# Performance work log

Hardware: AMD Instinct MI355X
Metric: run time of the kernel (lower is better)

## Reference

```python
import jax, jax.numpy as jnp
import numpy as np

B, S, D_IN, D_OUT = 4, 4096, 768, 768

def setup_inputs() -> dict:
    key = jax.random.key(0)
    k1, k2, k3, k4 = jax.random.split(key, 4)
    x = jax.random.normal(k1, (B, S, D_IN), dtype=jnp.float32)
    # Stored as [d_in, d_out]; torch Linear computes x @ W.T with W [d_out, d_in],
    # which is equivalent to x @ W_here for a fresh random init.
    Wq = jax.random.normal(k2, (D_IN, D_OUT), dtype=jnp.float32) * (1.0 / np.sqrt(D_IN))
    Wk = jax.random.normal(k3, (D_IN, D_OUT), dtype=jnp.float32) * (1.0 / np.sqrt(D_IN))
    Wv = jax.random.normal(k4, (D_IN, D_OUT), dtype=jnp.float32) * (1.0 / np.sqrt(D_IN))
    return {"x": x, "Wq": Wq, "Wk": Wk, "Wv": Wv}

def reference(x, Wq, Wk, Wv):
    # x: [B, S, d_in]
    q = jnp.einsum('bsi,io->bso', x, Wq)  # [B, S, d_out]
    k = jnp.einsum('bsi,io->bso', x, Wk)
    v = jnp.einsum('bsi,io->bso', x, Wv)
    scale = 1.0 / jnp.sqrt(jnp.asarray(q.shape[-1], dtype=q.dtype))
    scores = jnp.einsum('bqd,bkd->bqk', q, k)  # [B, S, S]
    S_len = scores.shape[-1]
    causal = jnp.tril(jnp.ones((S_len, S_len), dtype=bool))  # True = keep
    scores = jnp.where(causal[None, :, :], scores, -jnp.inf)
    weights = jax.nn.softmax(scores * scale, axis=-1)
    # dropout p=0.0 -> identity
    return jnp.einsum('bqk,bkd->bqd', weights, v)
```

## Files before the change

### kernel.cpp

```cpp
#include <hip/hip_runtime.h>

typedef __attribute__((ext_vector_type(8))) short short8;
typedef __attribute__((ext_vector_type(4))) float f32x4;
typedef unsigned short u16;

#define MFMA_BF16 __builtin_amdgcn_mfma_f32_16x16x32_bf16
#define S_BARRIER()  asm volatile("s_barrier" ::: "memory")
#define WAIT_LGKM0() asm volatile("s_waitcnt lgkmcnt(0)" ::: "memory")
#define WAIT_VM(n)   asm volatile("s_waitcnt vmcnt(" #n ")" ::: "memory")

__device__ __forceinline__ u16 f2bf(float f) {
    unsigned int u = __builtin_bit_cast(unsigned int, f);
    u = (u + 0x7FFFu + ((u >> 16) & 1u)) >> 16;
    return (u16)u;
}

__device__ __forceinline__ void gl_lds16(const void* g, void* l) {
    __builtin_amdgcn_global_load_lds(
        (const __attribute__((address_space(1))) unsigned int*)g,
        (__attribute__((address_space(3))) unsigned int*)l, 16, 0, 0);
}

constexpr int D = 768;
constexpr int S = 4096;
constexpr float SCALE = 0.03608439182435161f;

__device__ __forceinline__ void tri_decode(int t, int& i, int& j) {
    i = (int)((sqrtf(8.0f * t + 1.0f) - 1.0f) * 0.5f);
    while ((i + 1) * (i + 2) / 2 <= t) ++i;
    while (i * (i + 1) / 2 > t) --i;
    j = t - i * (i + 1) / 2;
}

template<int NCH, int NT>
__device__ __forceinline__ void stageT(const u16* __restrict__ g, u16* lds, int kcol, int tid) {
    #pragma unroll
    for (int i = 0; i < NCH; ++i) {
        const int ch = i * NT + tid;
        const int row = ch >> 3, c = ch & 7;
        const int cs = c ^ (row & 7);
        gl_lds16(g + (size_t)row * 768 + kcol + cs * 8, lds + ch * 8);
    }
}
__device__ __forceinline__ short8 ldsfrag(const u16* p, int row, int ks, int lane) {
    const int cs = (ks * 4 + (lane >> 4)) ^ (row & 7);
    return *reinterpret_cast<const short8*>(p + row * 64 + cs * 8);
}

__global__ __launch_bounds__(256)
void conv_x(const float* __restrict__ x, u16* __restrict__ xb) {
    const size_t i = ((size_t)blockIdx.x * 256 + threadIdx.x) * 4;
    const float4 v = *reinterpret_cast<const float4*>(x + i);
    ushort4 o;
    o.x = f2bf(v.x); o.y = f2bf(v.y); o.z = f2bf(v.z); o.w = f2bf(v.w);
    *reinterpret_cast<ushort4*>(xb + i) = o;
}

__global__ __launch_bounds__(256)
void conv_wt(const float* __restrict__ Wq, const float* __restrict__ Wk,
             const float* __restrict__ Wv, u16* __restrict__ WT) {
    __shared__ float t[64][65];
    const int tid = threadIdx.x;
    const int k0 = blockIdx.x * 64, n0 = blockIdx.y * 64, z = blockIdx.z;
    const float* __restrict__ W = (z == 0) ? Wq : ((z == 1) ? Wk : Wv);
    #pragma unroll
    for (int i = 0; i < 4; ++i) {
        const int e = (i * 256 + tid) * 4;
        const int r = e >> 6, c = e & 63;
        const float4 v = *reinterpret_cast<const float4*>(W + (size_t)(k0 + r) * D + n0 + c);
        t[r][c] = v.x; t[r][c + 1] = v.y; t[r][c + 2] = v.z; t[r][c + 3] = v.w;
    }
    __syncthreads();
    u16* O = WT + (size_t)z * D * D;
    #pragma unroll
    for (int i = 0; i < 4; ++i) {
        const int e = (i * 256 + tid) * 4;
        const int n = e >> 6, kq = e & 63;
        ushort4 o;
        o.x = f2bf(t[kq + 0][n]); o.y = f2bf(t[kq + 1][n]);
        o.z = f2bf(t[kq + 2][n]); o.w = f2bf(t[kq + 3][n]);
        *reinterpret_cast<ushort4*>(O + (size_t)(n0 + n) * D + k0 + kq) = o;
    }
}

__global__ __launch_bounds__(256, 2)
void qkv_gemm(const u16* __restrict__ xb, const u16* __restrict__ WT,
              u16* __restrict__ qo, u16* __restrict__ ko, u16* __restrict__ vt)
{
    __shared__ u16 smem[40960];
    u16* sAb = smem;
    u16* sBb = smem + 16384;
    const int tid = threadIdx.x, lane = tid & 63, w = tid >> 6;
    const int wr = w >> 1, wn = w & 1;
    const int bm = blockIdx.x * 128;
    const u16* __restrict__ A = xb + (size_t)bm * 768;
    const u16* __restrict__ B = WT + (size_t)blockIdx.y * 192 * 768;

    f32x4 acc[4][6] = {};

    stageT<4,256>(A, sAb, 0, tid);          stageT<6,256>(B, sBb, 0, tid);
    stageT<4,256>(A, sAb + 8192, 64, tid);  stageT<6,256>(B, sBb + 12288, 64, tid);
    WAIT_VM(10); S_BARRIER();

    #pragma unroll 2
    for (int kt = 0; kt < 12; ++kt) {
        const int cur = kt & 1;
        const u16* pA = sAb + cur * 8192;
        const u16* pB = sBb + cur * 12288;
        short8 a0[4], b0[6], a1[4], b1[6];
        #pragma unroll
        for (int fr = 0; fr < 4; ++fr) a0[fr] = ldsfrag(pA, wr * 64 + fr * 16 + (lane & 15), 0, lane);
        #pragma unroll
        for (int fc = 0; fc < 6; ++fc) b0[fc] = ldsfrag(pB, wn * 96 + fc * 16 + (lane & 15), 0, lane);
        #pragma unroll
        for (int fr = 0; fr < 4; ++fr)
            #pragma unroll
            for (int fc = 0; fc < 6; ++fc)
                acc[fr][fc] = MFMA_BF16(a0[fr], b0[fc], acc[fr][fc], 0, 0, 0);
        #pragma unroll
        for (int fr = 0; fr < 4; ++fr) a1[fr] = ldsfrag(pA, wr * 64 + fr * 16 + (lane & 15), 1, lane);
        #pragma unroll
        for (int fc = 0; fc < 6; ++fc) b1[fc] = ldsfrag(pB, wn * 96 + fc * 16 + (lane & 15), 1, lane);
        WAIT_LGKM0(); S_BARRIER();
        if (kt < 10) { stageT<4,256>(A, sAb + cur * 8192, (kt + 2) * 64, tid);
                       stageT<6,256>(B, sBb + cur * 12288, (kt + 2) * 64, tid); }
        __builtin_amdgcn_s_setprio(1);
        #pragma unroll
        for (int fr = 0; fr < 4; ++fr)
            #pragma unroll
            for (int fc = 0; fc < 6; ++fc)
                acc[fr][fc] = MFMA_BF16(a1[fr], b1[fc], acc[fr][fc], 0, 0, 0);
        __builtin_amdgcn_s_setprio(0);
        if (kt < 10) { WAIT_VM(10); } else { WAIT_VM(0); }
        S_BARRIER();
    }

    const int z = blockIdx.y >> 2, nb = (blockIdx.y & 3) * 192;
    if (z == 2) {
        u16* sT = smem;
        #pragma unroll
        for (int fr = 0; fr < 4; ++fr)
            #pragma unroll
            for (int fc = 0; fc < 6; ++fc) {
                const int n  = wn * 96 + fc * 16 + (lane & 15);
                const int mb = wr * 64 + fr * 16 + (lane >> 4) * 4;
                ushort4 pk;
                pk.x = f2bf(acc[fr][fc][0]); pk.y = f2bf(acc[fr][fc][1]);
                pk.z = f2bf(acc[fr][fc][2]); pk.w = f2bf(acc[fr][fc][3]);
                *reinterpret_cast<ushort4*>(&sT[n * 128 + (mb ^ ((n & 7) << 3))]) = pk;
            }
        __syncthreads();
        const int batch = bm >> 12, s_in = bm & 4095;
        u16* __restrict__ vdst = vt + ((size_t)batch * 768 + nb) * 4096 + s_in;
        #pragma unroll
        for (int v = 0; v < 12; ++v) {
            const int ch = v * 256 + tid;
            const int dd = ch >> 4, sc = ch & 15;
            const short8 o = *reinterpret_cast<const short8*>(
                &sT[dd * 128 + ((sc * 8) ^ ((dd & 7) << 3))]);
            *reinterpret_cast<short8*>(vdst + (size_t)dd * 4096 + sc * 8) = o;
        }
    } else {
        u16* __restrict__ dst = (z == 0) ? qo : ko;
        #pragma unroll
        for (int fr = 0; fr < 4; ++fr)
            #pragma unroll
            for (int fc = 0; fc < 6; ++fc)
                #pragma unroll
                for (int r = 0; r < 4; ++r) {
                    const int m = bm + wr * 64 + fr * 16 + (lane >> 4) * 4 + r;
                    const int n = nb + wn * 96 + fc * 16 + (lane & 15);
                    dst[(size_t)m * 768 + n] = f2bf(acc[fr][fc][r]);
                }
    }
}

__global__ __launch_bounds__(256, 2)
void qkt_gemm(const u16* __restrict__ Qg, const u16* __restrict__ Kg,
              u16* __restrict__ Pp, float* __restrict__ Lp)
{
    __shared__ u16 smem[32768];
    const int tid = threadIdx.x, lane = tid & 63, w = tid >> 6;
    const int wr = w >> 1, wn = w & 1;
    const int bx = blockIdx.x;
    const int bxs = (bx & 7) * 66 + (bx >> 3);
    int ti, tj;
    tri_decode(bxs, ti, tj);
    const int b = blockIdx.y;
    const u16* __restrict__ A = Qg + ((size_t)b * S + ti * 128) * 768;
    const u16* __restrict__ B = Kg + ((size_t)b * S + tj * 128) * 768;

    f32x4 acc[4][4] = {};

    stageT<4,256>(A, smem, 0, tid);           stageT<4,256>(B, smem + 16384, 0, tid);
    stageT<4,256>(A, smem + 8192, 64, tid);   stageT<4,256>(B, smem + 24576, 64, tid);
    WAIT_VM(8); S_BARRIER();

    #pragma unroll 2
    for (int kt = 0; kt < 12; ++kt) {
        const int cur = kt & 1;
        const u16* pA = smem + cur * 8192;
        const u16* pB = smem + 16384 + cur * 8192;
        short8 a0[4], b0[4], a1[4], b1[4];
        #pragma unroll
        for (int fr = 0; fr < 4; ++fr) a0[fr] = ldsfrag(pA, wr * 64 + fr * 16 + (lane & 15), 0, lane);
        #pragma unroll
        for (int fc = 0; fc < 4; ++fc) b0[fc] = ldsfrag(pB, wn * 64 + fc * 16 + (lane & 15), 0, lane);
        #pragma unroll
        for (int fr = 0; fr < 4; ++fr)
            #pragma unroll
            for (int fc = 0; fc < 4; ++fc)
                acc[fr][fc] = MFMA_BF16(a0[fr], b0[fc], acc[fr][fc], 0, 0, 0);
        #pragma unroll
        for (int fr = 0; fr < 4; ++fr) a1[fr] = ldsfrag(pA, wr * 64 + fr * 16 + (lane & 15), 1, lane);
        #pragma unroll
        for (int fc = 0; fc < 4; ++fc) b1[fc] = ldsfrag(pB, wn * 64 + fc * 16 + (lane & 15), 1, lane);
        WAIT_LGKM0(); S_BARRIER();
        if (kt < 10) { stageT<4,256>(A, smem + cur * 8192, (kt + 2) * 64, tid);
                       stageT<4,256>(B, smem + 16384 + cur * 8192, (kt + 2) * 64, tid); }
        __builtin_amdgcn_s_setprio(1);
        #pragma unroll
        for (int fr = 0; fr < 4; ++fr)
            #pragma unroll
            for (int fc = 0; fc < 4; ++fc)
                acc[fr][fc] = MFMA_BF16(a1[fr], b1[fc], acc[fr][fc], 0, 0, 0);
        __builtin_amdgcn_s_setprio(0);
        if (kt < 10) { WAIT_VM(8); } else { WAIT_VM(0); }
        S_BARRIER();
    }

    u16* sC = smem;
    const bool diag = (ti == tj);
    #pragma unroll
    for (int fr = 0; fr < 4; ++fr)
        #pragma unroll
        for (int r = 0; r < 4; ++r) {
            const int ml = wr * 64 + fr * 16 + (lane >> 4) * 4 + r;
            const int gm = ti * 128 + ml;
            float rs = 0.0f;
            #pragma unroll
            for (int fc = 0; fc < 4; ++fc) {
                const int nl = wn * 64 + fc * 16 + (lane & 15);
                float p = __expf(acc[fr][fc][r] * SCALE - 10.0f);
                if (diag && (tj * 128 + nl) > gm) p = 0.0f;
                rs += p;
                sC[ml * 132 + nl] = f2bf(p);
            }
            rs += __shfl_xor(rs, 1);
            rs += __shfl_xor(rs, 2);
            rs += __shfl_xor(rs, 4);
            rs += __shfl_xor(rs, 8);
            if ((lane & 15) == 0)
                Lp[((size_t)b * 64 + tj * 2 + wn) * 4096 + gm] = rs;
        }
    __syncthreads();
    u16* __restrict__ tbase = Pp + ((size_t)b * 528 + (size_t)ti * (ti + 1) / 2 + tj) * 16384;
    #pragma unroll
    for (int v = 0; v < 8; ++v) {
        const int ch = v * 256 + tid;
        const int row = ch >> 4, c = ch & 15;
        const short8 o = *reinterpret_cast<const short8*>(&sC[row * 132 + c * 8]);
        *reinterpret_cast<short8*>(tbase + row * 128 + c * 8) = o;
    }
}

__global__ __launch_bounds__(256)
void reduce_l(const float* __restrict__ Lp, float* __restrict__ Li)
{
    const int row = blockIdx.x * 256 + threadIdx.x;
    const int b = row >> 12, r = row & 4095;
    const int jm = 2 * (r >> 7) + 1;
    float l = 0.0f;
    for (int j = 0; j <= jm; ++j)
        l += Lp[((size_t)b * 64 + j) * 4096 + r];
    Li[row] = 1.0f / l;
}

__global__ __launch_bounds__(512)
void pv_gemm(const u16* __restrict__ Pp, const u16* __restrict__ Vt,
             const float* __restrict__ Li, float* __restrict__ out)
{
    __shared__ u16 sV[2][192 * 64];
    __shared__ u16 sP[2][128 * 64];
    const int tid  = threadIdx.x;
    const int lane = tid & 63;
    const int w    = tid >> 6;
    const int wq   = w >> 2;
    const int wd   = w & 3;
    const int bid  = blockIdx.x;
    const int rank = (bid < 256) ? bid : 767 - bid;
    const int i    = rank >> 4;
    const int b    = (rank >> 2) & 3;
    const int dq   = rank & 3;
    const int q0   = i * 128, d0 = dq * 192;
    const int nkt  = 2 * i + 2;
    const u16* __restrict__ Pt  = Pp + ((size_t)b * 528 + (size_t)i * (i + 1) / 2) * 16384;
    const u16* __restrict__ vtb = Vt + ((size_t)b * D + d0) * S;

    f32x4 acc[4][3] = {};

    auto stage_v = [&](int buf, int kt) {
        #pragma unroll
        for (int n = 0; n < 3; ++n) {
            const int ch  = n * 512 + tid;
            const int row = ch >> 3;
            const int csw = (ch & 7) ^ (row & 7);
            gl_lds16(vtb + (size_t)row * S + kt * 64 + csw * 8, &sV[buf][ch * 8]);
        }
    };
    auto stage_p = [&](int buf, int kt) {
        const u16* base = Pt + (size_t)(kt >> 1) * 16384 + (kt & 1) * 64;
        #pragma unroll
        for (int n = 0; n < 2; ++n) {
            const int ch  = n * 512 + tid;
            const int row = ch >> 3;
            const int csw = (ch & 7) ^ (row & 7);
            gl_lds16(base + row * 128 + csw * 8, &sP[buf][ch * 8]);
        }
    };

    stage_v(0, 0); stage_p(0, 0);
    __syncthreads();
    int cur = 0;
    for (int kt = 0; kt < nkt; ++kt) {
        if (kt + 1 < nkt) { stage_v(cur ^ 1, kt + 1); stage_p(cur ^ 1, kt + 1); }
        #pragma unroll
        for (int ks = 0; ks < 2; ++ks) {
            short8 a[4];
            #pragma unroll
            for (int fr = 0; fr < 4; ++fr) {
                const int row = wq * 64 + fr * 16 + (lane & 15);
                const int cch = (ks * 4 + (lane >> 4)) ^ (row & 7);
                a[fr] = *reinterpret_cast<const short8*>(&sP[cur][row * 64 + cch * 8]);
            }
            #pragma unroll
            for (int fc = 0; fc < 3; ++fc) {
                const int dr  = wd * 48 + fc * 16 + (lane & 15);
                const int vch = (ks * 4 + (lane >> 4)) ^ (dr & 7);
                const short8 bv = *reinterpret_cast<const short8*>(&sV[cur][dr * 64 + vch * 8]);
                #pragma unroll
                for (int fr = 0; fr < 4; ++fr)
                    acc[fr][fc] = MFMA_BF16(a[fr], bv, acc[fr][fc], 0, 0, 0);
            }
        }
        __syncthreads();
        cur ^= 1;
    }

    #pragma unroll
    for (int fr = 0; fr < 4; ++fr)
        #pragma unroll
        for (int rr = 0; rr < 4; ++rr) {
            const int row = q0 + wq * 64 + fr * 16 + (lane >> 4) * 4 + rr;
            const float linv = Li[b * 4096 + row];
            #pragma unroll
            for (int fc = 0; fc < 3; ++fc) {
                const int col = d0 + wd * 48 + fc * 16 + (lane & 15);
                out[((size_t)b * S + row) * D + col] = acc[fr][fc][rr] * linv;
            }
        }
}

extern "C" void kernel_launch(void* const* d_in, const int* in_sizes, int n_in,
                              void* d_out, int out_size, void* d_ws, size_t ws_size,
                              hipStream_t stream) {
    const float* x  = (const float*)d_in[0];
    const float* Wq = (const float*)d_in[1];
    const float* Wk = (const float*)d_in[2];
    const float* Wv = (const float*)d_in[3];
    float* out = (float*)d_out;

    const size_t SD = (size_t)16384 * 768;
    u16* q  = (u16*)d_ws;
    u16* k  = q  + SD;
    u16* vt = k  + SD;
    u16* xb = vt + SD;
    u16* WT = xb + SD;
    u16* Pp = WT + (size_t)3 * 768 * 768;
    float* Lp = (float*)(Pp + (size_t)4 * 528 * 16384);
    float* Li = Lp + (size_t)4 * 64 * 4096;
    (void)in_sizes; (void)n_in; (void)out_size; (void)ws_size;

    conv_x  <<<12288, 256, 0, stream>>>(x, xb);
    conv_wt <<<dim3(12, 12, 3), 256, 0, stream>>>(Wq, Wk, Wv, WT);
    qkv_gemm<<<dim3(128, 12), 256, 0, stream>>>(xb, WT, q, k, vt);
    qkt_gemm<<<dim3(528, 4), 256, 0, stream>>>(q, k, Pp, Lp);
    reduce_l<<<64, 256, 0, stream>>>(Lp, Li);
    pv_gemm <<<512, 512, 0, stream>>>(Pp, vt, Li, out);
}
```

Before: 254.6 us.

## Enlarge QK^T tiles to 256x256 with 8 waves and a four-slot LDS pipeline

The causal QK^T GEMM moves from 128x128 tiles with 4 waves to 256x256 tiles with 8 waves. This cuts the triangular grid from 528 to 136 blocks per batch and doubles operand reuse from LDS. The K loop now rotates through four 32-wide half-slices with swizzled global-to-LDS loads and split MFMA phases separated by barriers. Results are written back as 128x128 P tiles, with tiles above the diagonal skipped, and the row-sum bookkeeping in reduce_l is adjusted to match. In exchange, the diagonal 256 tiles compute masked work, there are many more barriers per iteration, and the larger LDS and register footprint may limit occupancy.

Measured after the change: 273.4 us. 1.07x slower.

```diff
diff --git a/kernel.cpp b/kernel.cpp
--- a/kernel.cpp
+++ b/kernel.cpp
@@ -175,92 +175,177 @@
     }
 }
 
-__global__ __launch_bounds__(256, 2)
+__global__ __launch_bounds__(512, 2)
 void qkt_gemm(const u16* __restrict__ Qg, const u16* __restrict__ Kg,
               u16* __restrict__ Pp, float* __restrict__ Lp)
 {
-    __shared__ u16 smem[32768];
+    __shared__ u16 smem[65536];
     const int tid = threadIdx.x, lane = tid & 63, w = tid >> 6;
-    const int wr = w >> 1, wn = w & 1;
+    const int wr = w >> 2, wn = w & 3;
     const int bx = blockIdx.x;
-    const int bxs = (bx & 7) * 66 + (bx >> 3);
+    const int bxs = (bx & 7) * 17 + (bx >> 3);
     int ti, tj;
     tri_decode(bxs, ti, tj);
     const int b = blockIdx.y;
-    const u16* __restrict__ A = Qg + ((size_t)b * S + ti * 128) * 768;
-    const u16* __restrict__ B = Kg + ((size_t)b * S + tj * 128) * 768;
-
-    f32x4 acc[4][4] = {};
-
-    stageT<4,256>(A, smem, 0, tid);           stageT<4,256>(B, smem + 16384, 0, tid);
-    stageT<4,256>(A, smem + 8192, 64, tid);   stageT<4,256>(B, smem + 24576, 64, tid);
+    const u16* __restrict__ Ag = Qg + ((size_t)b * S + ti * 256) * 768;
+    const u16* __restrict__ Bg = Kg + ((size_t)b * S + tj * 256) * 768;
+
+    u16* A00 = smem;            u16* A01 = smem + 8192;
+    u16* A10 = smem + 16384;    u16* A11 = smem + 24576;
+    u16* B00 = smem + 32768;    u16* B01 = smem + 40960;
+    u16* B10 = smem + 49152;    u16* B11 = smem + 57344;
+
+    f32x4 acc[8][4] = {};
+
+    auto stg = [&](const u16* __restrict__ g, u16* slot, int kt, int h) {
+        const int kk = (kt >= 12) ? kt - 12 : kt;
+        const int kcol = kk * 64 + h * 32;
+        #pragma unroll
+        for (int i = 0; i < 2; ++i) {
+            const int ch = i * 512 + tid;
+            const int row = ch >> 2, pc = ch & 3;
+            const int c = (pc - (row >> 1)) & 3;
+            gl_lds16(g + (size_t)row * 768 + kcol + c * 8, slot + ch * 8);
+        }
+    };
+    auto rdA = [&](const u16* s, int frb, short8* a) {
+        #pragma unroll
+        for (int fr = 0; fr < 4; ++fr) {
+            const int row = wr * 128 + (frb + fr) * 16 + (lane & 15);
+            const int pc = ((lane >> 4) + (row >> 1)) & 3;
+            a[fr] = *reinterpret_cast<const short8*>(s + row * 32 + pc * 8);
+        }
+    };
+    auto rdB = [&](const u16* s, short8* bb) {
+        #pragma unroll
+        for (int fc = 0; fc < 4; ++fc) {
+            const int row = wn * 64 + fc * 16 + (lane & 15);
+            const int pc = ((lane >> 4) + (row >> 1)) & 3;
+            bb[fc] = *reinterpret_cast<const short8*>(s + row * 32 + pc * 8);
+        }
+    };
+    auto mm = [&](short8* a, short8* bb, int frb) {
+        __builtin_amdgcn_s_setprio(1);
+        #pragma unroll
+        for (int fr = 0; fr < 4; ++fr)
+            #pragma unroll
+            for (int fc = 0; fc < 4; ++fc)
+                acc[frb + fr][fc] = MFMA_BF16(a[fr], bb[fc], acc[frb + fr][fc], 0, 0, 0);
+        __builtin_amdgcn_s_setprio(0);
+    };
+
+    stg(Ag, A00, 0, 0); stg(Bg, B00, 0, 0);
+    stg(Ag, A01, 0, 1); stg(Bg, B01, 0, 1);
+    stg(Ag, A10, 1, 0); stg(Bg, B10, 1, 0);
     WAIT_VM(8); S_BARRIER();
 
-    #pragma unroll 2
-    for (int kt = 0; kt < 12; ++kt) {
-        const int cur = kt & 1;
-        const u16* pA = smem + cur * 8192;
-        const u16* pB = smem + 16384 + cur * 8192;
-        short8 a0[4], b0[4], a1[4], b1[4];
-        #pragma unroll
-        for (int fr = 0; fr < 4; ++fr) a0[fr] = ldsfrag(pA, wr * 64 + fr * 16 + (lane & 15), 0, lane);
-        #pragma unroll
-        for (int fc = 0; fc < 4; ++fc) b0[fc] = ldsfrag(pB, wn * 64 + fc * 16 + (lane & 15), 0, lane);
-        #pragma unroll
-        for (int fr = 0; fr < 4; ++fr)
-            #pragma unroll
-            for (int fc = 0; fc < 4; ++fc)
-                acc[fr][fc] = MFMA_BF16(a0[fr], b0[fc], acc[fr][fc], 0, 0, 0);
-        #pragma unroll
-        for (int fr = 0; fr < 4; ++fr) a1[fr] = ldsfrag(pA, wr * 64 + fr * 16 + (lane & 15), 1, lane);
-        #pragma unroll
-        for (int fc = 0; fc < 4; ++fc) b1[fc] = ldsfrag(pB, wn * 64 + fc * 16 + (lane & 15), 1, lane);
-        WAIT_LGKM0(); S_BARRIER();
-        if (kt < 10) { stageT<4,256>(A, smem + cur * 8192, (kt + 2) * 64, tid);
-                       stageT<4,256>(B, smem + 16384 + cur * 8192, (kt + 2) * 64, tid); }
-        __builtin_amdgcn_s_setprio(1);
-        #pragma unroll
-        for (int fr = 0; fr < 4; ++fr)
-            #pragma unroll
-            for (int fc = 0; fc < 4; ++fc)
-                acc[fr][fc] = MFMA_BF16(a1[fr], b1[fc], acc[fr][fc], 0, 0, 0);
-        __builtin_amdgcn_s_setprio(0);
-        if (kt < 10) { WAIT_VM(8); } else { WAIT_VM(0); }
-        S_BARRIER();
-    }
-
-    u16* sC = smem;
+    short8 a[4], bb[4];
+    #pragma unroll 1
+    for (int t = 0; t < 6; ++t) {
+        const int ka = 2 * t, kb = 2 * t + 1;
+        WAIT_VM(4);
+        rdA(A00, 0, a); rdB(B00, bb);
+        stg(Ag, A11, kb, 1);
+        S_BARRIER();
+        mm(a, bb, 0);
+        S_BARRIER();
+        rdA(A00, 4, a);
+        stg(Bg, B11, kb, 1);
+        S_BARRIER();
+        mm(a, bb, 4);
+        S_BARRIER();
+        WAIT_VM(4);
+        rdA(A01, 0, a); rdB(B01, bb);
+        stg(Ag, A00, ka + 2, 0);
+        S_BARRIER();
+        mm(a, bb, 0);
+        S_BARRIER();
+        rdA(A01, 4, a);
+        stg(Bg, B00, ka + 2, 0);
+        S_BARRIER();
+        mm(a, bb, 4);
+        S_BARRIER();
+        WAIT_VM(4);
+        rdA(A10, 0, a); rdB(B10, bb);
+        stg(Ag, A01, ka + 2, 1);
+        S_BARRIER();
+        mm(a, bb, 0);
+        S_BARRIER();
+        rdA(A10, 4, a);
+        stg(Bg, B01, ka + 2, 1);
+        S_BARRIER();
+        mm(a, bb, 4);
+        S_BARRIER();
+        WAIT_VM(4);
+        rdA(A11, 0, a); rdB(B11, bb);
+        stg(Ag, A10, kb + 2, 0);
+        S_BARRIER();
+        mm(a, bb, 0);
+        S_BARRIER();
+        rdA(A11, 4, a);
+        stg(Bg, B10, kb + 2, 0);
+        S_BARRIER();
+        mm(a, bb, 4);
+        S_BARRIER();
+    }
+    WAIT_VM(0); S_BARRIER();
+
     const bool diag = (ti == tj);
     #pragma unroll
-    for (int fr = 0; fr < 4; ++fr)
+    for (int fr = 0; fr < 8; ++fr)
         #pragma unroll
         for (int r = 0; r < 4; ++r) {
-            const int ml = wr * 64 + fr * 16 + (lane >> 4) * 4 + r;
-            const int gm = ti * 128 + ml;
+            const int ml = wr * 128 + fr * 16 + (lane >> 4) * 4 + r;
+            const int gm = ti * 256 + ml;
             float rs = 0.0f;
             #pragma unroll
             for (int fc = 0; fc < 4; ++fc) {
                 const int nl = wn * 64 + fc * 16 + (lane & 15);
                 float p = __expf(acc[fr][fc][r] * SCALE - 10.0f);
-                if (diag && (tj * 128 + nl) > gm) p = 0.0f;
+                if (diag && (tj * 256 + nl) > gm) p = 0.0f;
+                acc[fr][fc][r] = p;
                 rs += p;
-                sC[ml * 132 + nl] = f2bf(p);
             }
             rs += __shfl_xor(rs, 1);
             rs += __shfl_xor(rs, 2);
             rs += __shfl_xor(rs, 4);
             rs += __shfl_xor(rs, 8);
             if ((lane & 15) == 0)
-                Lp[((size_t)b * 64 + tj * 2 + wn) * 4096 + gm] = rs;
-        }
-    __syncthreads();
-    u16* __restrict__ tbase = Pp + ((size_t)b * 528 + (size_t)ti * (ti + 1) / 2 + tj) * 16384;
-    #pragma unroll
-    for (int v = 0; v < 8; ++v) {
-        const int ch = v * 256 + tid;
-        const int row = ch >> 4, c = ch & 15;
-        const short8 o = *reinterpret_cast<const short8*>(&sC[row * 132 + c * 8]);
-        *reinterpret_cast<short8*>(tbase + row * 128 + c * 8) = o;
+                Lp[((size_t)b * 64 + tj * 4 + wn) * 4096 + gm] = rs;
+        }
+
+    u16* sC = smem;
+    #pragma unroll
+    for (int half = 0; half < 2; ++half) {
+        if (wr == half) {
+            #pragma unroll
+            for (int fr = 0; fr < 8; ++fr)
+                #pragma unroll
+                for (int fc = 0; fc < 4; ++fc)
+                    #pragma unroll
+                    for (int r = 0; r < 4; ++r) {
+                        const int mr = fr * 16 + (lane >> 4) * 4 + r;
+                        const int nl = wn * 64 + fc * 16 + (lane & 15);
+                        sC[mr * 260 + nl] = f2bf(acc[fr][fc][r]);
+                    }
+        }
+        __syncthreads();
+        const int i128 = ti * 2 + half;
+        #pragma unroll
+        for (int jh = 0; jh < 2; ++jh) {
+            const int j128 = tj * 2 + jh;
+            if (j128 <= i128) {
+                u16* __restrict__ tb = Pp + ((size_t)b * 528 + (size_t)i128 * (i128 + 1) / 2 + j128) * 16384;
+                #pragma unroll
+                for (int v = 0; v < 4; ++v) {
+                    const int ch = v * 512 + tid;
+                    const int row = ch >> 4, c = ch & 15;
+                    const short8 o = *reinterpret_cast<const short8*>(&sC[row * 260 + jh * 128 + c * 8]);
+                    *reinterpret_cast<short8*>(tb + row * 128 + c * 8) = o;
+                }
+            }
+        }
+        __syncthreads();
     }
 }
 
@@ -269,7 +354,7 @@
 {
     const int row = blockIdx.x * 256 + threadIdx.x;
     const int b = row >> 12, r = row & 4095;
-    const int jm = 2 * (r >> 7) + 1;
+    const int jm = (r >> 6) | 3;
     float l = 0.0f;
     for (int j = 0; j <= jm; ++j)
         l += Lp[((size_t)b * 64 + j) * 4096 + r];
@@ -384,7 +469,7 @@
     conv_x  <<<12288, 256, 0, stream>>>(x, xb);
     conv_wt <<<dim3(12, 12, 3), 256, 0, stream>>>(Wq, Wk, Wv, WT);
     qkv_gemm<<<dim3(128, 12), 256, 0, stream>>>(xb, WT, q, k, vt);
-    qkt_gemm<<<dim3(528, 4), 256, 0, stream>>>(q, k, Pp, Lp);
+    qkt_gemm<<<dim3(136, 4), 512, 0, stream>>>(q, k, Pp, Lp);
     reduce_l<<<64, 256, 0, stream>>>(Lp, Li);
     pv_gemm <<<512, 512, 0, stream>>>(Pp, vt, Li, out);
 }
```
